# Kernel optimization log

Hardware: AMD Instinct MI355X
Metric: run time of the kernel (lower is better)

## Reference

```python
import jax, jax.numpy as jnp
import numpy as np

V = np.array([[1.0, 1.0, 1.0], [1.0, -1.0, 1.0], [1.0, 1.0, -1.0]], dtype=np.float32)


def _lin_combs(kernels: np.ndarray) -> np.ndarray:
    """Project (O, C, 3, 3) kernels onto inverse of the 9x9 GCK +/-1 basis.
    Returns (O, C*9) with layout c*9 + (3*i + j), matching the torch module."""
    O, C = kernels.shape[0], kernels.shape[1]
    # basis_flat[k=3i+j, p=3r+s] = V[i,r] * V[j,s]
    basis_flat = np.einsum('ir,js->ijrs', V, V).reshape(9, 9)
    basis_inv = np.linalg.inv(basis_flat)
    kflat = kernels.reshape(O, C, 9)
    comb = np.einsum('kp,ocp->ock', basis_inv, kflat)  # (O, C, 9)
    return np.ascontiguousarray(comb.reshape(O, C * 9))


def setup_inputs() -> dict:
    key = jax.random.key(0)
    k1, k2 = jax.random.split(key)
    B, C, O, H, W = 1, 64, 64, 514, 514
    x = jax.random.normal(k1, (B, C, H, W), dtype=jnp.float32)
    kernels = np.asarray(jax.random.normal(k2, (O, C, 3, 3), dtype=jnp.float32))
    linCombs = jnp.asarray(_lin_combs(kernels))  # (O, C*9)
    return {"input": x, "linCombs": linCombs}


def reference(input, linCombs):
    # GCK 3x3 conv: rowwise +/-1 stage -> colwise +/-1 stage -> linComb matmul.
    x = input
    B, C, H, W = x.shape
    O = linCombs.shape[0]
    Ho, Wo = H - 2, W - 2  # padding = 0
    Vj = jnp.asarray(V)
    # rowwise stage: convolve (cross-correlate) along rows with each +/-1 vector
    rows = jnp.stack([x[:, :, r:r + Ho, :] for r in range(3)])       # (3,B,C,Ho,W)
    rowwise = jnp.einsum('ir,rbchw->bcihw', Vj, rows)                 # (B,C,3,Ho,W)
    # colwise stage: convolve along columns with each +/-1 vector
    cols = jnp.stack([rowwise[..., s:s + Wo] for s in range(3)])      # (3,B,C,3,Ho,Wo)
    colwise = jnp.einsum('js,sbcihw->bcijhw', Vj, cols)               # (B,C,3,3,Ho,Wo)
    feats = colwise.reshape(B, C * 9, Ho * Wo)                        # k = c*9 + 3i + j
    out = jnp.einsum('ok,bkp->bop', linCombs, feats)
    return out.reshape(B, O, Ho, Wo)
```

## Files before the change

### kernel.cpp

```cpp
#include <hip/hip_runtime.h>
#include <hip/hip_bf16.h>


constexpr int kC = 64, kO = 64;
constexpr int kH = 514, kW = 514;
constexpr int kHO = 512, kWO = 512;
constexpr int kNPIX = kH * kW;

typedef __attribute__((ext_vector_type(8))) short short8;
typedef __attribute__((ext_vector_type(4))) float floatx4;

__device__ inline unsigned short f2bf(float f) {
    unsigned int u = __float_as_uint(f);
    unsigned int r = (u + 0x7fffu + ((u >> 16) & 1u)) >> 16;
    return (unsigned short)r;
}

__global__ void gck_wprep(const float* __restrict__ lin, unsigned short* __restrict__ w2) {
    int t = blockIdx.x * 256 + threadIdx.x;
    if (t >= kO * kC * 9) return;
    int tap = t % 9;
    int c   = (t / 9) % kC;
    int o   = t / (9 * kC);
    int r = tap / 3, s = tap % 3;
    const float Vm[3][3] = {{1.f, 1.f, 1.f}, {1.f, -1.f, 1.f}, {1.f, 1.f, -1.f}};
    float acc = 0.f;
#pragma unroll
    for (int i = 0; i < 3; i++)
#pragma unroll
        for (int j = 0; j < 3; j++)
            acc += lin[o * (kC * 9) + c * 9 + 3 * i + j] * Vm[i][r] * Vm[j][s];
    int kglob = tap * 64 + c;
    int ks = kglob >> 5, kg = (kglob >> 3) & 3, e = kglob & 7;
    w2[((ks * 4 + kg) * 64 + o) * 8 + e] = f2bf(acc);
}

__global__ __launch_bounds__(256, 3) void gck_conv(const float* __restrict__ x,
                                                   const unsigned short* __restrict__ w2,
                                                   float* __restrict__ out) {
    __shared__ unsigned short xs[6 * 66 * 64];

    const int bid = blockIdx.x;
    const int ct = bid & 7;
    const int rt = bid >> 3;
    const int hbase = rt * 4;
    const int wbase = ct * 64;
    const int t    = threadIdx.x;
    const int wave = t >> 6;
    const int lane = t & 63;
    const int l16  = lane & 15;
    const int kg   = lane >> 4;

    {
        const int q    = t & 15;
        const int cg4  = t >> 4;
        const int ch0  = cg4 * 4;
        const int colb = q * 4;
#pragma unroll
        for (int r = 0; r < 6; ++r) {
            const float* gp = x + (hbase + r) * kW + wbase + colb;
            float v[4][4];
            if ((r & 1) == 0) {
#pragma unroll
                for (int c = 0; c < 4; ++c) {
                    float4 f = *reinterpret_cast<const float4*>(gp + (ch0 + c) * kNPIX);
                    v[c][0] = f.x; v[c][1] = f.y; v[c][2] = f.z; v[c][3] = f.w;
                }
            } else {
#pragma unroll
                for (int c = 0; c < 4; ++c) {
                    float2 f0 = *reinterpret_cast<const float2*>(gp + (ch0 + c) * kNPIX);
                    float2 f1 = *reinterpret_cast<const float2*>(gp + (ch0 + c) * kNPIX + 2);
                    v[c][0] = f0.x; v[c][1] = f0.y; v[c][2] = f1.x; v[c][3] = f1.y;
                }
            }
#pragma unroll
            for (int j = 0; j < 4; ++j) {
                int col = colb + j;
                ushort4 u4;
                u4.x = f2bf(v[0][j]); u4.y = f2bf(v[1][j]);
                u4.z = f2bf(v[2][j]); u4.w = f2bf(v[3][j]);
                int addr = (r * 66 + col) * 64 + (((cg4 >> 1) ^ (col & 7)) * 8) + (cg4 & 1) * 4;
                *reinterpret_cast<ushort4*>(&xs[addr]) = u4;
            }
        }
#pragma unroll
        for (int j = 0; j < 3; ++j) {
            int idx = j * 256 + t;
            int col = 64 + (idx & 1);
            int ch  = (idx >> 1) & 63;
            int r   = idx >> 7;
            float f = x[ch * kNPIX + (hbase + r) * kW + wbase + col];
            int addr = (r * 66 + col) * 64 + ((ch >> 3) ^ (col & 7)) * 8 + (ch & 7);
            xs[addr] = f2bf(f);
        }
    }
    __syncthreads();

    floatx4 acc[4][4];
#pragma unroll
    for (int m = 0; m < 4; m++)
#pragma unroll
        for (int n = 0; n < 4; n++) acc[m][n] = (floatx4){0.f, 0.f, 0.f, 0.f};

    const short8* w2v = reinterpret_cast<const short8*>(w2);

    short8 a_cur[4];
#pragma unroll
    for (int m = 0; m < 4; m++) a_cur[m] = w2v[(0 * 4 + kg) * 64 + m * 16 + l16];

#pragma unroll 2
    for (int ks = 0; ks < 18; ++ks) {
        int tap = ks >> 1;
        int r0  = tap / 3;
        int s   = tap - r0 * 3;

        short8 a_nxt[4];
        int ksn = (ks < 17) ? ks + 1 : ks;
#pragma unroll
        for (int m = 0; m < 4; m++) a_nxt[m] = w2v[(ksn * 4 + kg) * 64 + m * 16 + l16];

        int rr = wave + r0;
        int u  = (ks & 1) * 4 + kg;
        short8 b[4];
#pragma unroll
        for (int n = 0; n < 4; ++n) {
            int col  = n * 16 + l16 + s;
            int addr = (rr * 66 + col) * 64 + ((u ^ (col & 7)) * 8);
            b[n] = *reinterpret_cast<const short8*>(&xs[addr]);
        }

#pragma unroll
        for (int m = 0; m < 4; m++)
#pragma unroll
            for (int n = 0; n < 4; n++)
                acc[m][n] = __builtin_amdgcn_mfma_f32_16x16x32_bf16(a_cur[m], b[n], acc[m][n], 0, 0, 0);

#pragma unroll
        for (int m = 0; m < 4; m++) a_cur[m] = a_nxt[m];
    }

    const int h = hbase + wave;
#pragma unroll
    for (int m = 0; m < 4; m++) {
#pragma unroll
        for (int n = 0; n < 4; n++) {
            int wcol = wbase + n * 16 + l16;
#pragma unroll
            for (int j = 0; j < 4; j++) {
                int o = m * 16 + kg * 4 + j;
                out[(o * kHO + h) * kWO + wcol] = acc[m][n][j];
            }
        }
    }
}

extern "C" void kernel_launch(void* const* d_in, const int* in_sizes, int n_in,
                              void* d_out, int out_size, void* d_ws, size_t ws_size,
                              hipStream_t stream) {
    const float* x   = (const float*)d_in[0];
    const float* lin = (const float*)d_in[1];
    float* out = (float*)d_out;

    unsigned short* w2 = (unsigned short*)d_ws;

    gck_wprep<<<(kO * kC * 9 + 255) / 256, 256, 0, stream>>>(lin, w2);
    gck_conv<<<(kHO / 4) * 8, 256, 0, stream>>>(x, w2, out);
}
```

Measured before the change: 138.7 us.

## Stream input rows through a ring buffer with register-resident weights

Replaces the one-shot tile kernel (4 rows x 64 cols, 2048 blocks) with a persistent-style kernel in which each block covers 8 output rows x 128 columns. Input rows stream through a 4-slot LDS ring, and the next row is prefetched into registers while the MFMAs for the current row run. All 18 k-slices of weights are held in registers per wave, and the XCD-aware block mapping along with a new double-XOR swizzle aims to cut halo reloads and LDS bank conflicts. In exchange, register pressure is much higher (occupancy drops to 2 blocks per CU), only 256 blocks are launched, and two barriers are added per row.

```diff
diff --git a/kernel.cpp b/kernel.cpp
--- a/kernel.cpp
+++ b/kernel.cpp
@@ -6,6 +6,11 @@
 constexpr int kH = 514, kW = 514;
 constexpr int kHO = 512, kWO = 512;
 constexpr int kNPIX = kH * kW;
+
+constexpr int TPX   = 128;
+constexpr int TROWS = 8;
+constexpr int LCOLS = 130;
+constexpr int SLOT  = LCOLS * 64;
 
 typedef __attribute__((ext_vector_type(8))) short short8;
 typedef __attribute__((ext_vector_type(4))) float floatx4;
@@ -35,123 +40,136 @@
     w2[((ks * 4 + kg) * 64 + o) * 8 + e] = f2bf(acc);
 }
 
-__global__ __launch_bounds__(256, 3) void gck_conv(const float* __restrict__ x,
-                                                   const unsigned short* __restrict__ w2,
-                                                   float* __restrict__ out) {
-    __shared__ unsigned short xs[6 * 66 * 64];
+__device__ inline void stage_load(const float* __restrict__ x, int grow, int wbase,
+                                  int q, int cg, int t, float (&v)[8][4], float& ev) {
+    const float* gp = x + (size_t)grow * kW + wbase + q * 4;
+    const int ch0 = cg * 8;
+    if ((grow & 1) == 0) {
+#pragma unroll
+        for (int c = 0; c < 8; ++c) {
+            float4 f = *reinterpret_cast<const float4*>(gp + (size_t)(ch0 + c) * kNPIX);
+            v[c][0] = f.x; v[c][1] = f.y; v[c][2] = f.z; v[c][3] = f.w;
+        }
+    } else {
+#pragma unroll
+        for (int c = 0; c < 8; ++c) {
+            const float* p = gp + (size_t)(ch0 + c) * kNPIX;
+            float2 f0 = *reinterpret_cast<const float2*>(p);
+            float2 f1 = *reinterpret_cast<const float2*>(p + 2);
+            v[c][0] = f0.x; v[c][1] = f0.y; v[c][2] = f1.x; v[c][3] = f1.y;
+        }
+    }
+    if (t < 128) {
+        int ch = t & 63, col = 128 + (t >> 6);
+        ev = x[(size_t)ch * kNPIX + (size_t)grow * kW + wbase + col];
+    }
+}
+
+__device__ inline void stage_write(unsigned short* xs, int slot_row, int q, int cg, int t,
+                                   const float (&v)[8][4], float ev) {
+#pragma unroll
+    for (int j = 0; j < 4; ++j) {
+        int col = q * 4 + j;
+        short8 u8;
+#pragma unroll
+        for (int c = 0; c < 8; ++c) u8[c] = (short)f2bf(v[c][j]);
+        int swz = (cg ^ (col & 7) ^ ((col >> 3) & 7)) & 7;
+        *reinterpret_cast<short8*>(&xs[(slot_row * LCOLS + col) * 64 + swz * 8]) = u8;
+    }
+    if (t < 128) {
+        int ch = t & 63, col = 128 + (t >> 6);
+        int swz = ((ch >> 3) ^ (col & 7) ^ ((col >> 3) & 7)) & 7;
+        xs[(slot_row * LCOLS + col) * 64 + swz * 8 + (ch & 7)] = f2bf(ev);
+    }
+}
+
+__global__ __launch_bounds__(256, 2) void gck_stream(const float* __restrict__ x,
+                                                     const unsigned short* __restrict__ w2,
+                                                     float* __restrict__ out) {
+    __shared__ unsigned short xs[4 * SLOT];
 
     const int bid = blockIdx.x;
-    const int ct = bid & 7;
-    const int rt = bid >> 3;
-    const int hbase = rt * 4;
-    const int wbase = ct * 64;
+    const int xcd = bid & 7, jj = bid >> 3;
+    const int ct = xcd & 3;
+    const int rt = (xcd >> 2) * 32 + jj;
+    const int wbase = ct * TPX;
+    const int hbase = rt * TROWS;
+
     const int t    = threadIdx.x;
     const int wave = t >> 6;
     const int lane = t & 63;
     const int l16  = lane & 15;
     const int kg   = lane >> 4;
+    const int o0   = (wave & 1) * 32;
+    const int px0  = (wave >> 1) * 64;
 
-    {
-        const int q    = t & 15;
-        const int cg4  = t >> 4;
-        const int ch0  = cg4 * 4;
-        const int colb = q * 4;
+    const int q  = t & 31;
+    const int cg = t >> 5;
+
+    const short8* w2v = reinterpret_cast<const short8*>(w2);
+    short8 a[18][2];
 #pragma unroll
-        for (int r = 0; r < 6; ++r) {
-            const float* gp = x + (hbase + r) * kW + wbase + colb;
-            float v[4][4];
-            if ((r & 1) == 0) {
+    for (int ks = 0; ks < 18; ++ks)
 #pragma unroll
-                for (int c = 0; c < 4; ++c) {
-                    float4 f = *reinterpret_cast<const float4*>(gp + (ch0 + c) * kNPIX);
-                    v[c][0] = f.x; v[c][1] = f.y; v[c][2] = f.z; v[c][3] = f.w;
-                }
-            } else {
+        for (int m = 0; m < 2; ++m)
+            a[ks][m] = w2v[(ks * 4 + kg) * 64 + o0 + m * 16 + l16];
+
+    float v[8][4]; float ev = 0.f;
 #pragma unroll
-                for (int c = 0; c < 4; ++c) {
-                    float2 f0 = *reinterpret_cast<const float2*>(gp + (ch0 + c) * kNPIX);
-                    float2 f1 = *reinterpret_cast<const float2*>(gp + (ch0 + c) * kNPIX + 2);
-                    v[c][0] = f0.x; v[c][1] = f0.y; v[c][2] = f1.x; v[c][3] = f1.y;
-                }
-            }
-#pragma unroll
-            for (int j = 0; j < 4; ++j) {
-                int col = colb + j;
-                ushort4 u4;
-                u4.x = f2bf(v[0][j]); u4.y = f2bf(v[1][j]);
-                u4.z = f2bf(v[2][j]); u4.w = f2bf(v[3][j]);
-                int addr = (r * 66 + col) * 64 + (((cg4 >> 1) ^ (col & 7)) * 8) + (cg4 & 1) * 4;
-                *reinterpret_cast<ushort4*>(&xs[addr]) = u4;
-            }
-        }
-#pragma unroll
-        for (int j = 0; j < 3; ++j) {
-            int idx = j * 256 + t;
-            int col = 64 + (idx & 1);
-            int ch  = (idx >> 1) & 63;
-            int r   = idx >> 7;
-            float f = x[ch * kNPIX + (hbase + r) * kW + wbase + col];
-            int addr = (r * 66 + col) * 64 + ((ch >> 3) ^ (col & 7)) * 8 + (ch & 7);
-            xs[addr] = f2bf(f);
-        }
+    for (int r = 0; r < 3; ++r) {
+        stage_load(x, hbase + r, wbase, q, cg, t, v, ev);
+        stage_write(xs, r, q, cg, t, v, ev);
     }
     __syncthreads();
 
-    floatx4 acc[4][4];
+    floatx4 acc[2][4];
 #pragma unroll
-    for (int m = 0; m < 4; m++)
+    for (int m = 0; m < 2; m++)
 #pragma unroll
         for (int n = 0; n < 4; n++) acc[m][n] = (floatx4){0.f, 0.f, 0.f, 0.f};
 
-    const short8* w2v = reinterpret_cast<const short8*>(w2);
+    for (int i = 0; i < TROWS; ++i) {
+        const bool pf = (i + 3 < 10);
+        if (pf) stage_load(x, hbase + i + 3, wbase, q, cg, t, v, ev);
 
-    short8 a_cur[4];
 #pragma unroll
-    for (int m = 0; m < 4; m++) a_cur[m] = w2v[(0 * 4 + kg) * 64 + m * 16 + l16];
-
-#pragma unroll 2
-    for (int ks = 0; ks < 18; ++ks) {
-        int tap = ks >> 1;
-        int r0  = tap / 3;
-        int s   = tap - r0 * 3;
-
-        short8 a_nxt[4];
-        int ksn = (ks < 17) ? ks + 1 : ks;
+        for (int ks = 0; ks < 18; ++ks) {
+            const int tap = ks >> 1;
+            const int tr  = tap / 3;
+            const int s   = tap - tr * 3;
+            const int u   = (ks & 1) * 4 + kg;
+            const int srow = (i + tr) & 3;
+            short8 b[4];
 #pragma unroll
-        for (int m = 0; m < 4; m++) a_nxt[m] = w2v[(ksn * 4 + kg) * 64 + m * 16 + l16];
-
-        int rr = wave + r0;
-        int u  = (ks & 1) * 4 + kg;
-        short8 b[4];
+            for (int n = 0; n < 4; ++n) {
+                int col = px0 + n * 16 + l16 + s;
+                int swz = (u ^ (col & 7) ^ ((col >> 3) & 7)) & 7;
+                b[n] = *reinterpret_cast<const short8*>(&xs[(srow * LCOLS + col) * 64 + swz * 8]);
+            }
 #pragma unroll
-        for (int n = 0; n < 4; ++n) {
-            int col  = n * 16 + l16 + s;
-            int addr = (rr * 66 + col) * 64 + ((u ^ (col & 7)) * 8);
-            b[n] = *reinterpret_cast<const short8*>(&xs[addr]);
+            for (int m = 0; m < 2; ++m)
+#pragma unroll
+                for (int n = 0; n < 4; ++n)
+                    acc[m][n] = __builtin_amdgcn_mfma_f32_16x16x32_bf16(a[ks][m], b[n], acc[m][n], 0, 0, 0);
         }
 
+        const int h = hbase + i;
 #pragma unroll
-        for (int m = 0; m < 4; m++)
+        for (int m = 0; m < 2; ++m)
 #pragma unroll
-            for (int n = 0; n < 4; n++)
-                acc[m][n] = __builtin_amdgcn_mfma_f32_16x16x32_bf16(a_cur[m], b[n], acc[m][n], 0, 0, 0);
+            for (int n = 0; n < 4; ++n) {
+                int col = wbase + px0 + n * 16 + l16;
+#pragma unroll
+                for (int j = 0; j < 4; ++j) {
+                    int o = o0 + m * 16 + kg * 4 + j;
+                    out[((size_t)o * kHO + h) * kWO + col] = acc[m][n][j];
+                }
+                acc[m][n] = (floatx4){0.f, 0.f, 0.f, 0.f};
+            }
 
-#pragma unroll
-        for (int m = 0; m < 4; m++) a_cur[m] = a_nxt[m];
-    }
-
-    const int h = hbase + wave;
-#pragma unroll
-    for (int m = 0; m < 4; m++) {
-#pragma unroll
-        for (int n = 0; n < 4; n++) {
-            int wcol = wbase + n * 16 + l16;
-#pragma unroll
-            for (int j = 0; j < 4; j++) {
-                int o = m * 16 + kg * 4 + j;
-                out[(o * kHO + h) * kWO + wcol] = acc[m][n][j];
-            }
-        }
+        __syncthreads();
+        if (pf) stage_write(xs, (i + 3) & 3, q, cg, t, v, ev);
+        __syncthreads();
     }
 }
 
@@ -165,5 +183,5 @@
     unsigned short* w2 = (unsigned short*)d_ws;
 
     gck_wprep<<<(kO * kC * 9 + 255) / 256, 256, 0, stream>>>(lin, w2);
-    gck_conv<<<(kHO / 4) * 8, 256, 0, stream>>>(x, w2, out);
+    gck_stream<<<256, 256, 0, stream>>>(x, w2, out);
 }
```

Measured after the change: 185.6 us. 1.34x slower.
